# Optimization experiments

Hardware: AMD Instinct MI355X
Metric: run time of the kernel (lower is better)

## Reference

```python
import jax, jax.numpy as jnp
import numpy as np

DIM = 1024
NUM_HEADS = 16
HEAD_DIM = DIM // NUM_HEADS
SCALE = HEAD_DIM ** -0.5


def setup_inputs() -> dict:
    key = jax.random.key(0)
    k1, k2, k3 = jax.random.split(key, 3)
    B, N = 2, 2048
    x = jax.random.normal(k1, (B, N, DIM), dtype=jnp.float32)
    W_qkv = jax.random.normal(k2, (DIM, 3 * DIM), dtype=jnp.float32) * (DIM ** -0.5)
    b_qkv = jnp.zeros((3 * DIM,), dtype=jnp.float32)
    W_proj = jax.random.normal(k3, (DIM, DIM), dtype=jnp.float32) * (DIM ** -0.5)
    b_proj = jnp.zeros((DIM,), dtype=jnp.float32)
    return {"x": x, "W_qkv": W_qkv, "b_qkv": b_qkv, "W_proj": W_proj, "b_proj": b_proj}


def reference(x, W_qkv, b_qkv, W_proj, b_proj):
    B, N, D = x.shape
    qkv = x @ W_qkv + b_qkv                      # [B, N, 3D]
    qkv = qkv.reshape(B, N, 3, NUM_HEADS, HEAD_DIM)
    qkv = jnp.transpose(qkv, (2, 0, 3, 1, 4))    # [3, B, H, N, hd]
    q, k, v = qkv[0], qkv[1], qkv[2]
    attn = jnp.einsum('bhqd,bhkd->bhqk', q, k) * SCALE  # [B, H, N, N]
    attn = jax.nn.softmax(attn, axis=-1)
    out = jnp.einsum('bhqk,bhkd->bhqd', attn, v)        # [B, H, N, hd]
    out = jnp.transpose(out, (0, 2, 1, 3)).reshape(B, N, D)
    out = out @ W_proj + b_proj
    return out
```

## Files before the change

kernel.cpp:

```cpp
#include <hip/hip_runtime.h>


typedef __bf16 bf16_t;
typedef __bf16 bf16x2 __attribute__((ext_vector_type(2)));
typedef __bf16 bf16x4 __attribute__((ext_vector_type(4)));
typedef __bf16 bf16x8 __attribute__((ext_vector_type(8)));
typedef float  f32x4  __attribute__((ext_vector_type(4)));

#define NTOK 2048
#define DIM  1024
#define NH   16
#define HD   64
#define SCL2 0.18033688011112042f

#define MFMA16(a, b, c) __builtin_amdgcn_mfma_f32_16x16x32_bf16((a), (b), (c), 0, 0, 0)
#define BAR()   __builtin_amdgcn_s_barrier()
#define LGKM0() asm volatile("s_waitcnt lgkmcnt(0)" ::: "memory")

__device__ __forceinline__ void gload_lds16(const void* g, void* l) {
  __builtin_amdgcn_global_load_lds((const __attribute__((address_space(1))) void*)g,
                                   (__attribute__((address_space(3))) void*)l, 16, 0, 0);
}

__device__ __forceinline__ void transpose_cvt_tile(const float* __restrict__ W,
                                                   bf16_t* __restrict__ WT,
                                                   int cols, int bx, int by) {
  __shared__ float tile[32][33];
  int j0 = bx * 32, i0 = by * 32;
  int c = threadIdx.x & 31, r0 = threadIdx.x >> 5;
#pragma unroll
  for (int it = 0; it < 4; ++it) {
    int r = r0 + it * 8;
    tile[r][c] = W[(long)(i0 + r) * cols + j0 + c];
  }
  __syncthreads();
#pragma unroll
  for (int it = 0; it < 4; ++it) {
    int r = r0 + it * 8;
    int orow = j0 + r, ocol = i0 + c;
    WT[(long)orow * 1024 + ((((ocol >> 3) ^ (orow & 7)) << 3) | (ocol & 7))] =
        (bf16_t)tile[c][r];
  }
}

__global__ __launch_bounds__(256) void k_prep(const float* __restrict__ x,
                                              bf16_t* __restrict__ xb,
                                              const float* __restrict__ Wq,
                                              bf16_t* __restrict__ WqT,
                                              const float* __restrict__ Wp,
                                              bf16_t* __restrict__ WpT) {
  int id = blockIdx.x;
  if (id < 2048) {
    int i = (id * 256 + threadIdx.x) * 8;
    float4 a = *(const float4*)(x + i);
    float4 b = *(const float4*)(x + i + 4);
    bf16x8 v;
    v[0] = (bf16_t)a.x; v[1] = (bf16_t)a.y; v[2] = (bf16_t)a.z; v[3] = (bf16_t)a.w;
    v[4] = (bf16_t)b.x; v[5] = (bf16_t)b.y; v[6] = (bf16_t)b.z; v[7] = (bf16_t)b.w;
    int r = i >> 10, c = (i & 1023) >> 3;
    *(bf16x8*)(xb + r * 1024 + ((c ^ (r & 7)) << 3)) = v;
  } else if (id < 2048 + 3072) {
    int t = id - 2048;
    transpose_cvt_tile(Wq, WqT, 3072, t % 96, t / 96);
  } else {
    int t = id - 5120;
    transpose_cvt_tile(Wp, WpT, 1024, t & 31, t >> 5);
  }
}

__global__ __launch_bounds__(512, 2) void k_gemm_qkv(const bf16_t* __restrict__ xb,
                                                     const bf16_t* __restrict__ WqT,
                                                     const float* __restrict__ bq,
                                                     bf16_t* __restrict__ Qb,
                                                     bf16_t* __restrict__ Kb,
                                                     bf16_t* __restrict__ Vt) {
  __shared__ alignas(16) bf16_t SH[65536];
  const int t = threadIdx.x;
  const int w = t >> 6, lane = t & 63;
  const int l15 = lane & 15, g = lane >> 4;
  const int wm = w >> 2, wn = w & 3;
  const int xr = l15 & 7;

  const int bid = blockIdx.x;
  const int xcd = bid & 7, ib = bid >> 3;
  const int bm = ((xcd & 3) * 4 + (ib & 3)) * 256;
  const int bn = ((xcd >> 2) * 6 + (ib >> 2)) * 256;

  const bf16_t* Ag = xb + (long)bm * 1024;
  const bf16_t* Bg = WqT + (long)bn * 1024;

  auto Asl = [&](int slot) -> bf16_t* { return SH + slot * 16384; };
  auto Bsl = [&](int slot) -> bf16_t* { return SH + 32768 + slot * 16384; };

  auto st1 = [&](bf16_t* lds, const bf16_t* gsrc, int row0, int kt) {
    gload_lds16(gsrc + (long)(row0 + (t >> 3)) * 1024 + kt * 64 + (t & 7) * 8,
                (char*)lds + row0 * 128 + t * 16);
  };
  auto evA = [&](int slot, int kt, int half) {
    st1(Asl(slot), Ag, half * 64, kt);
    st1(Asl(slot), Ag, half * 64 + 128, kt);
  };
  auto evB = [&](int slot, int kt, int half) {
    st1(Bsl(slot), Bg, half * 128, kt);
    st1(Bsl(slot), Bg, half * 128 + 64, kt);
  };

  f32x4 acc[8][4];
  const f32x4 vzero = {0.f, 0.f, 0.f, 0.f};
#pragma unroll
  for (int m = 0; m < 8; ++m)
#pragma unroll
    for (int n = 0; n < 4; ++n) acc[m][n] = vzero;

  bf16x8 bf[4][2], af[4][2];
  auto ldB2 = [&](int slot, int n0) {
#pragma unroll
    for (int n = n0; n < n0 + 2; ++n)
#pragma unroll
      for (int kk = 0; kk < 2; ++kk)
        bf[n][kk] = *(const bf16x8*)((const char*)Bsl(slot) +
                    (wn * 64 + n * 16 + l15) * 128 + (((kk * 4 + g) ^ xr) << 4));
  };
  auto ldA = [&](int slot, int half) {
#pragma unroll
    for (int m = 0; m < 4; ++m)
#pragma unroll
      for (int kk = 0; kk < 2; ++kk)
        af[m][kk] = *(const bf16x8*)((const char*)Asl(slot) +
                    (wm * 128 + half * 64 + m * 16 + l15) * 128 +
                    (((kk * 4 + g) ^ xr) << 4));
  };
  auto mma = [&](int mb, int nb) {
    __builtin_amdgcn_s_setprio(1);
#pragma unroll
    for (int m = 0; m < 4; ++m)
#pragma unroll
      for (int n = 0; n < 2; ++n)
#pragma unroll
        for (int kk = 0; kk < 2; ++kk)
          acc[mb + m][nb + n] = MFMA16(af[m][kk], bf[nb + n][kk], acc[mb + m][nb + n]);
    __builtin_amdgcn_s_setprio(0);
  };

  evB(0, 0, 0); evB(0, 0, 1); evA(0, 0, 0); evA(0, 0, 1);
  evB(1, 1, 0); evB(1, 1, 1); evA(1, 1, 0); evA(1, 1, 1);
  asm volatile("s_waitcnt vmcnt(8)" ::: "memory");
  BAR();

  for (int T = 0; T < 16; ++T) {
    const int h = T & 1;
    const bool stg = (T + 2) < 16;
    ldB2(h, 0); ldA(h, 0);
    BAR(); LGKM0();
    mma(0, 0);
    BAR();
    ldB2(h, 2);
    BAR(); LGKM0();
    mma(0, 2);
    BAR();
    ldA(h, 1);
    if (stg) { evB(h, T + 2, 0); evB(h, T + 2, 1); }
    BAR(); LGKM0();
    mma(4, 0);
    BAR();
    if (stg) {
      evA(h, T + 2, 0); evA(h, T + 2, 1);
      asm volatile("s_waitcnt vmcnt(8)" ::: "memory");
    } else {
      asm volatile("s_waitcnt vmcnt(0)" ::: "memory");
    }
    BAR();
    mma(4, 2);
    BAR();
  }

  const int t3 = bn >> 10;
  const int h0 = (bn & 1023) >> 6;
  const int bb = bm >> 11;
  const int tok0 = bm & 2047;
  {
    const int region = wn * 16384;
#pragma unroll
    for (int n = 0; n < 4; ++n) {
      int d = n * 16 + l15;
      float bias = bq[bn + wn * 64 + n * 16 + l15];
#pragma unroll
      for (int m = 0; m < 8; ++m) {
#pragma unroll
        for (int r = 0; r < 4; ++r) {
          int ltok = wm * 128 + m * 16 + g * 4 + r;
          float val = acc[m][n][r] + bias;
          int off;
          if (t3 == 0) {
            off = ltok * 64 + d;
            val *= SCL2;
          } else if (t3 == 1) {
            int rr = ltok & 63;
            off = (ltok >> 6) * 4096 + rr * 64 + (((d >> 3) ^ (rr & 7)) << 3) + (d & 7);
          } else {
            int ct = ltok & 63;
            off = (ltok >> 6) * 4096 + d * 64 + (((ct >> 3) ^ (d & 7)) << 3) + (ct & 7);
          }
          SH[region + off] = (bf16_t)val;
        }
      }
    }
  }
  BAR();
  bf16_t* dst = (t3 == 0) ? Qb : (t3 == 1 ? Kb : Vt);
  const long tilebase = (t3 == 0) ? (long)tok0 * HD : (long)(tok0 >> 6) * 4096;
#pragma unroll
  for (int hl = 0; hl < 4; ++hl) {
    long gbase = (long)(bb * NH + h0 + hl) * (NTOK * HD) + tilebase;
#pragma unroll
    for (int p = 0; p < 4; ++p) {
      bf16x8 vv = *(const bf16x8*)(SH + hl * 16384 + p * 4096 + t * 8);
      *(bf16x8*)(dst + gbase + p * 4096 + t * 8) = vv;
    }
  }
}

__device__ __forceinline__ void gemm_core(const bf16_t* __restrict__ A,
                                          const bf16_t* __restrict__ B,
                                          int K, int bm, int bn,
                                          bf16_t* As, bf16_t* Bs, f32x4 acc[4][4]) {
  const int t = threadIdx.x;
  const int lane = t & 63;
  const int w = t >> 6;
  const int wr = (w >> 1) * 64, wc = (w & 1) * 64;
  const int l15 = lane & 15, g = lane >> 4;
  const int srow = t >> 3, scol = (t & 7) * 8;
  const f32x4 vzero = {0.f, 0.f, 0.f, 0.f};
#pragma unroll
  for (int m = 0; m < 4; ++m)
#pragma unroll
    for (int n = 0; n < 4; ++n) acc[m][n] = vzero;

  const bf16_t* ga = A + (long)(bm + srow) * K + scol;
  const bf16_t* gb = B + (long)(bn + srow) * K + scol;
  bf16_t* lA = As + srow * 64 + scol;
  bf16_t* lB = Bs + srow * 64 + scol;
  const int xr = l15 & 7;

  auto stageAB = [&](int buf, int k0) {
#pragma unroll
    for (int j = 0; j < 4; ++j) {
      gload_lds16(ga + (long)32 * j * K + k0, lA + buf * 8192 + j * 2048);
      gload_lds16(gb + (long)32 * j * K + k0, lB + buf * 8192 + j * 2048);
    }
  };

  const int nsteps = K >> 6;
  stageAB(0, 0);
  stageAB(1, 64);

  for (int s = 0; s < nsteps; ++s) {
    if (s == nsteps - 1) asm volatile("s_waitcnt vmcnt(0)" ::: "memory");
    else                 asm volatile("s_waitcnt vmcnt(8)" ::: "memory");
    __builtin_amdgcn_s_barrier();
    const char* Ab = (const char*)(As + (s & 1) * 8192);
    const char* Bb = (const char*)(Bs + (s & 1) * 8192);
#pragma unroll
    for (int kk = 0; kk < 2; ++kk) {
      bf16x8 af[4], bfv[4];
#pragma unroll
      for (int m = 0; m < 4; ++m)
        af[m] = *(const bf16x8*)(Ab + (wr + m * 16 + l15) * 128 +
                                 (((kk * 4 + g) ^ xr) << 4));
#pragma unroll
      for (int n = 0; n < 4; ++n)
        bfv[n] = *(const bf16x8*)(Bb + (wc + n * 16 + l15) * 128 +
                                  (((kk * 4 + g) ^ xr) << 4));
#pragma unroll
      for (int m = 0; m < 4; ++m)
#pragma unroll
        for (int n = 0; n < 4; ++n)
          acc[m][n] = MFMA16(af[m], bfv[n], acc[m][n]);
    }
    __builtin_amdgcn_s_barrier();
    if (s + 2 < nsteps) stageAB(s & 1, (s + 2) * 64);
  }
}

__global__ __launch_bounds__(256, 3) void k_attn(const bf16_t* __restrict__ Qb,
                                                 const bf16_t* __restrict__ Kb,
                                                 const bf16_t* __restrict__ Vt,
                                                 bf16_t* __restrict__ Ob) {
  __shared__ alignas(16) bf16_t Ks[2][64 * 64];
  __shared__ alignas(16) bf16_t Vs[2][64 * 64];
  __shared__ alignas(16) char  P2[4][4096];

  const int b0 = blockIdx.x;
  const int swz = (b0 & 7) * 64 + (b0 >> 3);
  const int qt = swz & 15, bh = swz >> 4;
  const int b = bh >> 4, h = bh & 15;
  const int t = threadIdx.x;
  const int w = t >> 6, lane = t & 63;
  const int l15 = lane & 15, g = lane >> 4;
  const bf16_t* Qp = Qb + bh * (NTOK * HD);
  const bf16_t* Kp = Kb + bh * (NTOK * HD);
  const bf16_t* Vp = Vt + bh * (NTOK * HD);
  const int q0 = qt * 128 + w * 32;
  char* P2w = &P2[w][0];

  const int cs0 = ((g ^ (l15 & 7)) << 4);
  const int cs1 = cs0 ^ 64;

  bf16x8 qfr[2][2];
#pragma unroll
  for (int qf = 0; qf < 2; ++qf)
#pragma unroll
    for (int kk = 0; kk < 2; ++kk)
      qfr[qf][kk] = *(const bf16x8*)(Qp + (q0 + qf * 16 + l15) * HD + kk * 32 + g * 8);

  bf16x8 ones;
#pragma unroll
  for (int i = 0; i < 8; ++i) ones[i] = (bf16_t)1.0f;

  const f32x4 vzero = {0.f, 0.f, 0.f, 0.f};
  f32x4 o[2][4];
#pragma unroll
  for (int qf = 0; qf < 2; ++qf)
#pragma unroll
    for (int df = 0; df < 4; ++df) o[qf][df] = vzero;
  f32x4 o_sum[2] = {vzero, vzero};

  auto stage = [&](int buf, int tile) {
    const bf16_t* gk = Kp + tile * 4096 + t * 8;
    const bf16_t* gv = Vp + tile * 4096 + t * 8;
    gload_lds16(gk,        (char*)Ks[buf] + t * 16);
    gload_lds16(gk + 2048, (char*)Ks[buf] + 4096 + t * 16);
    gload_lds16(gv,        (char*)Vs[buf] + t * 16);
    gload_lds16(gv + 2048, (char*)Vs[buf] + 4096 + t * 16);
  };

  stage(0, 0);
  stage(1, 1);

  for (int i = 0; i < 32; ++i) {
    if (i == 31) asm volatile("s_waitcnt vmcnt(0)" ::: "memory");
    else         asm volatile("s_waitcnt vmcnt(4)" ::: "memory");
    __builtin_amdgcn_s_barrier();
    const char* kbuf = (const char*)Ks[i & 1];
    const char* vbuf = (const char*)Vs[i & 1];
    f32x4 s[2][4];
    __builtin_amdgcn_s_setprio(1);
#pragma unroll
    for (int kf = 0; kf < 4; ++kf) {
      int rb = (kf * 16 + l15) * 128;
      bf16x8 ka0 = *(const bf16x8*)(kbuf + rb + cs0);
      bf16x8 ka1 = *(const bf16x8*)(kbuf + rb + cs1);
      s[0][kf] = MFMA16(ka0, qfr[0][0], vzero);
      s[1][kf] = MFMA16(ka0, qfr[1][0], vzero);
      s[0][kf] = MFMA16(ka1, qfr[0][1], s[0][kf]);
      s[1][kf] = MFMA16(ka1, qfr[1][1], s[1][kf]);
    }
    __builtin_amdgcn_s_setprio(0);
#pragma unroll
    for (int qf = 0; qf < 2; ++qf)
#pragma unroll
      for (int kf = 0; kf < 4; ++kf) {
        bf16x4 pw;
        pw[0] = (bf16_t)__builtin_amdgcn_exp2f(s[qf][kf][0]);
        pw[1] = (bf16_t)__builtin_amdgcn_exp2f(s[qf][kf][1]);
        pw[2] = (bf16_t)__builtin_amdgcn_exp2f(s[qf][kf][2]);
        pw[3] = (bf16_t)__builtin_amdgcn_exp2f(s[qf][kf][3]);
        *(bf16x4*)(P2w + qf * 2048 + (2 * kf + (g >> 1)) * 256 + l15 * 16 + 8 * (g & 1)) = pw;
      }
    __builtin_amdgcn_s_setprio(1);
#pragma unroll
    for (int kb = 0; kb < 2; ++kb) {
      bf16x8 pf0 = *(const bf16x8*)(P2w + kb * 1024 + lane * 16);
      bf16x8 pf1 = *(const bf16x8*)(P2w + 2048 + kb * 1024 + lane * 16);
      int csk = kb ? cs1 : cs0;
      o_sum[0] = MFMA16(ones, pf0, o_sum[0]);
      o_sum[1] = MFMA16(ones, pf1, o_sum[1]);
#pragma unroll
      for (int df = 0; df < 4; ++df) {
        bf16x8 va = *(const bf16x8*)(vbuf + (df * 16 + l15) * 128 + csk);
        o[0][df] = MFMA16(va, pf0, o[0][df]);
        o[1][df] = MFMA16(va, pf1, o[1][df]);
      }
    }
    __builtin_amdgcn_s_setprio(0);
    __builtin_amdgcn_s_barrier();
    if (i + 2 < 32) stage(i & 1, i + 2);
  }
#pragma unroll
  for (int qf = 0; qf < 2; ++qf) {
    float inv = 1.0f / o_sum[qf][0];
    int tok = q0 + qf * 16 + l15;
    bf16_t* oprow = Ob + (long)(b * NTOK + tok) * DIM;
    const int xr = l15 & 7;
#pragma unroll
    for (int df = 0; df < 4; ++df) {
#pragma unroll
      for (int rp = 0; rp < 2; ++rp) {
        bf16x2 v2;
        v2[0] = (bf16_t)(o[qf][df][rp * 2]     * inv);
        v2[1] = (bf16_t)(o[qf][df][rp * 2 + 1] * inv);
        int c = h * 8 + df * 2 + (g >> 1);
        *(bf16x2*)(oprow + ((c ^ xr) << 3) + (g & 1) * 4 + rp * 2) = v2;
      }
    }
  }
}

__global__ __launch_bounds__(256) void k_gemm_proj(const bf16_t* __restrict__ Ob,
                                                   const bf16_t* __restrict__ WpT,
                                                   const float* __restrict__ bp,
                                                   float* __restrict__ out) {
  __shared__ alignas(16) bf16_t As[2 * 128 * 64];
  __shared__ alignas(16) bf16_t Bs[2 * 128 * 64];
  f32x4 acc[4][4];
  const int bid = blockIdx.x;
  const int bn = (bid & 7) * 128;
  const int bm = (bid >> 3) * 128;
  gemm_core(Ob, WpT, DIM, bm, bn, As, Bs, acc);

  const int lane = threadIdx.x & 63, w = threadIdx.x >> 6;
  const int wr = (w >> 1) * 64, wc = (w & 1) * 64;
  const int l15 = lane & 15, g = lane >> 4;
#pragma unroll
  for (int n = 0; n < 4; ++n) {
    int col = bn + wc + n * 16 + l15;
    float bias = bp[col];
#pragma unroll
    for (int m = 0; m < 4; ++m) {
      int rowb = bm + wr + m * 16 + g * 4;
#pragma unroll
      for (int r = 0; r < 4; ++r)
        out[(long)(rowb + r) * DIM + col] = acc[m][n][r] + bias;
    }
  }
}

extern "C" void kernel_launch(void* const* d_in, const int* in_sizes, int n_in,
                              void* d_out, int out_size, void* d_ws, size_t ws_size,
                              hipStream_t stream) {
  const float* x     = (const float*)d_in[0];
  const float* Wqkv  = (const float*)d_in[1];
  const float* bqkv  = (const float*)d_in[2];
  const float* Wproj = (const float*)d_in[3];
  const float* bproj = (const float*)d_in[4];
  float* out = (float*)d_out;

  char* ws = (char*)d_ws;
  bf16_t* xb  = (bf16_t*)(ws);
  bf16_t* WqT = (bf16_t*)(ws + (8l  << 20));
  bf16_t* WpT = (bf16_t*)(ws + (14l << 20));
  bf16_t* Qb  = (bf16_t*)(ws + (16l << 20));
  bf16_t* Kb  = (bf16_t*)(ws + (24l << 20));
  bf16_t* Vt  = (bf16_t*)(ws + (32l << 20));
  bf16_t* Ob  = (bf16_t*)(ws);

  k_prep<<<6144, 256, 0, stream>>>(x, xb, Wqkv, WqT, Wproj, WpT);
  k_gemm_qkv<<<192, 512, 0, stream>>>(xb, WqT, bqkv, Qb, Kb, Vt);
  k_attn<<<512, 256, 0, stream>>>(Qb, Kb, Vt, Ob);
  k_gemm_proj<<<256, 256, 0, stream>>>(Ob, WpT, bproj, out);
}
```

Baseline: 112.5 us.

## Retile QKV GEMM to 256x192 blocks for 256 workgroups across CUs

Changes the QKV projection GEMM tile from 256x256 to 256x192 so the grid grows from 192 to 256 workgroups, filling all 256 CUs in one wave instead of leaving some idle. The B tile shrinks to three 64-row chunks. The A prefetch is split into two halves issued at different points in the loop, with matching vmcnt waits. The epilogue now works out the Q/K/V target and head per 64-column sub-tile, since a 192-wide tile can span multiple heads and tensors. The trade-off is lower arithmetic intensity per block and a more intricate prefetch schedule.

```diff
diff --git a/kernel.cpp b/kernel.cpp
--- a/kernel.cpp
+++ b/kernel.cpp
@@ -74,7 +74,7 @@
                                                      bf16_t* __restrict__ Qb,
                                                      bf16_t* __restrict__ Kb,
                                                      bf16_t* __restrict__ Vt) {
-  __shared__ alignas(16) bf16_t SH[65536];
+  __shared__ alignas(16) bf16_t SH[57344];
   const int t = threadIdx.x;
   const int w = t >> 6, lane = t & 63;
   const int l15 = lane & 15, g = lane >> 4;
@@ -84,42 +84,45 @@
   const int bid = blockIdx.x;
   const int xcd = bid & 7, ib = bid >> 3;
   const int bm = ((xcd & 3) * 4 + (ib & 3)) * 256;
-  const int bn = ((xcd >> 2) * 6 + (ib >> 2)) * 256;
+  const int bn = ((xcd >> 2) * 8 + (ib >> 2)) * 192;
 
   const bf16_t* Ag = xb + (long)bm * 1024;
   const bf16_t* Bg = WqT + (long)bn * 1024;
 
   auto Asl = [&](int slot) -> bf16_t* { return SH + slot * 16384; };
-  auto Bsl = [&](int slot) -> bf16_t* { return SH + 32768 + slot * 16384; };
+  auto Bsl = [&](int slot) -> bf16_t* { return SH + 32768 + slot * 12288; };
 
   auto st1 = [&](bf16_t* lds, const bf16_t* gsrc, int row0, int kt) {
     gload_lds16(gsrc + (long)(row0 + (t >> 3)) * 1024 + kt * 64 + (t & 7) * 8,
                 (char*)lds + row0 * 128 + t * 16);
   };
-  auto evA = [&](int slot, int kt, int half) {
-    st1(Asl(slot), Ag, half * 64, kt);
-    st1(Asl(slot), Ag, half * 64 + 128, kt);
-  };
-  auto evB = [&](int slot, int kt, int half) {
-    st1(Bsl(slot), Bg, half * 128, kt);
-    st1(Bsl(slot), Bg, half * 128 + 64, kt);
-  };
-
-  f32x4 acc[8][4];
+  auto evA0 = [&](int slot, int kt) {
+    st1(Asl(slot), Ag, 0, kt);
+    st1(Asl(slot), Ag, 128, kt);
+  };
+  auto evA1 = [&](int slot, int kt) {
+    st1(Asl(slot), Ag, 64, kt);
+    st1(Asl(slot), Ag, 192, kt);
+  };
+  auto evB = [&](int slot, int kt) {
+    st1(Bsl(slot), Bg, 0, kt);
+    st1(Bsl(slot), Bg, 64, kt);
+    st1(Bsl(slot), Bg, 128, kt);
+  };
+
+  f32x4 acc[8][3];
   const f32x4 vzero = {0.f, 0.f, 0.f, 0.f};
 #pragma unroll
   for (int m = 0; m < 8; ++m)
 #pragma unroll
-    for (int n = 0; n < 4; ++n) acc[m][n] = vzero;
-
-  bf16x8 bf[4][2], af[4][2];
-  auto ldB2 = [&](int slot, int n0) {
-#pragma unroll
-    for (int n = n0; n < n0 + 2; ++n)
-#pragma unroll
-      for (int kk = 0; kk < 2; ++kk)
-        bf[n][kk] = *(const bf16x8*)((const char*)Bsl(slot) +
-                    (wn * 64 + n * 16 + l15) * 128 + (((kk * 4 + g) ^ xr) << 4));
+    for (int n = 0; n < 3; ++n) acc[m][n] = vzero;
+
+  bf16x8 bf[3][2], af[4][2];
+  auto ldBn = [&](int slot, int n) {
+#pragma unroll
+    for (int kk = 0; kk < 2; ++kk)
+      bf[n][kk] = *(const bf16x8*)((const char*)Bsl(slot) +
+                  (wn * 48 + n * 16 + l15) * 128 + (((kk * 4 + g) ^ xr) << 4));
   };
   auto ldA = [&](int slot, int half) {
 #pragma unroll
@@ -130,7 +133,7 @@
                     (wm * 128 + half * 64 + m * 16 + l15) * 128 +
                     (((kk * 4 + g) ^ xr) << 4));
   };
-  auto mma = [&](int mb, int nb) {
+  auto mma2 = [&](int mb) {
     __builtin_amdgcn_s_setprio(1);
 #pragma unroll
     for (int m = 0; m < 4; ++m)
@@ -138,80 +141,92 @@
       for (int n = 0; n < 2; ++n)
 #pragma unroll
         for (int kk = 0; kk < 2; ++kk)
-          acc[mb + m][nb + n] = MFMA16(af[m][kk], bf[nb + n][kk], acc[mb + m][nb + n]);
+          acc[mb + m][n] = MFMA16(af[m][kk], bf[n][kk], acc[mb + m][n]);
     __builtin_amdgcn_s_setprio(0);
   };
-
-  evB(0, 0, 0); evB(0, 0, 1); evA(0, 0, 0); evA(0, 0, 1);
-  evB(1, 1, 0); evB(1, 1, 1); evA(1, 1, 0); evA(1, 1, 1);
-  asm volatile("s_waitcnt vmcnt(8)" ::: "memory");
+  auto mma1 = [&](int mb) {
+    __builtin_amdgcn_s_setprio(1);
+#pragma unroll
+    for (int m = 0; m < 4; ++m)
+#pragma unroll
+      for (int kk = 0; kk < 2; ++kk)
+        acc[mb + m][2] = MFMA16(af[m][kk], bf[2][kk], acc[mb + m][2]);
+    __builtin_amdgcn_s_setprio(0);
+  };
+
+  evB(0, 0); evA0(0, 0); evA1(0, 0);
+  evB(1, 1); evA0(1, 1);
+  asm volatile("s_waitcnt vmcnt(5)" ::: "memory");
   BAR();
 
   for (int T = 0; T < 16; ++T) {
     const int h = T & 1;
     const bool stg = (T + 2) < 16;
-    ldB2(h, 0); ldA(h, 0);
+    if (T + 1 < 16) evA1(h ^ 1, T + 1);
+    ldBn(h, 0); ldBn(h, 1); ldA(h, 0);
     BAR(); LGKM0();
-    mma(0, 0);
+    mma2(0);
     BAR();
-    ldB2(h, 2);
+    ldBn(h, 2);
     BAR(); LGKM0();
-    mma(0, 2);
+    mma1(0);
     BAR();
     ldA(h, 1);
-    if (stg) { evB(h, T + 2, 0); evB(h, T + 2, 1); }
+    if (stg) evB(h, T + 2);
     BAR(); LGKM0();
-    mma(4, 0);
+    mma2(4);
     BAR();
     if (stg) {
-      evA(h, T + 2, 0); evA(h, T + 2, 1);
-      asm volatile("s_waitcnt vmcnt(8)" ::: "memory");
+      evA0(h, T + 2);
+      asm volatile("s_waitcnt vmcnt(5)" ::: "memory");
     } else {
       asm volatile("s_waitcnt vmcnt(0)" ::: "memory");
     }
     BAR();
-    mma(4, 2);
+    mma1(4);
     BAR();
   }
 
-  const int t3 = bn >> 10;
-  const int h0 = (bn & 1023) >> 6;
   const int bb = bm >> 11;
   const int tok0 = bm & 2047;
-  {
-    const int region = wn * 16384;
-#pragma unroll
-    for (int n = 0; n < 4; ++n) {
-      int d = n * 16 + l15;
-      float bias = bq[bn + wn * 64 + n * 16 + l15];
-#pragma unroll
-      for (int m = 0; m < 8; ++m) {
-#pragma unroll
-        for (int r = 0; r < 4; ++r) {
-          int ltok = wm * 128 + m * 16 + g * 4 + r;
-          float val = acc[m][n][r] + bias;
-          int off;
-          if (t3 == 0) {
-            off = ltok * 64 + d;
-            val *= SCL2;
-          } else if (t3 == 1) {
-            int rr = ltok & 63;
-            off = (ltok >> 6) * 4096 + rr * 64 + (((d >> 3) ^ (rr & 7)) << 3) + (d & 7);
-          } else {
-            int ct = ltok & 63;
-            off = (ltok >> 6) * 4096 + d * 64 + (((ct >> 3) ^ (d & 7)) << 3) + (ct & 7);
-          }
-          SH[region + off] = (bf16_t)val;
+#pragma unroll
+  for (int n = 0; n < 3; ++n) {
+    int lc = wn * 48 + n * 16 + l15;
+    int col = bn + lc;
+    int t3 = col >> 10;
+    int d = col & 63;
+    int region = lc >> 6;
+    float bias = bq[col];
+#pragma unroll
+    for (int m = 0; m < 8; ++m) {
+#pragma unroll
+      for (int r = 0; r < 4; ++r) {
+        int ltok = wm * 128 + m * 16 + g * 4 + r;
+        float val = acc[m][n][r] + bias;
+        int off;
+        if (t3 == 0) {
+          off = ltok * 64 + d;
+          val *= SCL2;
+        } else if (t3 == 1) {
+          int rr = ltok & 63;
+          off = (ltok >> 6) * 4096 + rr * 64 + (((d >> 3) ^ (rr & 7)) << 3) + (d & 7);
+        } else {
+          int ct = ltok & 63;
+          off = (ltok >> 6) * 4096 + d * 64 + (((ct >> 3) ^ (d & 7)) << 3) + (ct & 7);
         }
+        SH[region * 16384 + off] = (bf16_t)val;
       }
     }
   }
   BAR();
-  bf16_t* dst = (t3 == 0) ? Qb : (t3 == 1 ? Kb : Vt);
-  const long tilebase = (t3 == 0) ? (long)tok0 * HD : (long)(tok0 >> 6) * 4096;
-#pragma unroll
-  for (int hl = 0; hl < 4; ++hl) {
-    long gbase = (long)(bb * NH + h0 + hl) * (NTOK * HD) + tilebase;
+#pragma unroll
+  for (int hl = 0; hl < 3; ++hl) {
+    int col0 = bn + hl * 64;
+    int t3 = col0 >> 10;
+    int hh = (col0 >> 6) & 15;
+    bf16_t* dst = (t3 == 0) ? Qb : (t3 == 1 ? Kb : Vt);
+    long tilebase = (t3 == 0) ? (long)tok0 * HD : (long)(tok0 >> 6) * 4096;
+    long gbase = (long)(bb * NH + hh) * (NTOK * HD) + tilebase;
 #pragma unroll
     for (int p = 0; p < 4; ++p) {
       bf16x8 vv = *(const bf16x8*)(SH + hl * 16384 + p * 4096 + t * 8);
@@ -455,7 +470,7 @@
   bf16_t* Ob  = (bf16_t*)(ws);
 
   k_prep<<<6144, 256, 0, stream>>>(x, xb, Wqkv, WqT, Wproj, WpT);
-  k_gemm_qkv<<<192, 512, 0, stream>>>(xb, WqT, bqkv, Qb, Kb, Vt);
+  k_gemm_qkv<<<256, 512, 0, stream>>>(xb, WqT, bqkv, Qb, Kb, Vt);
   k_attn<<<512, 256, 0, stream>>>(Qb, Kb, Vt, Ob);
   k_gemm_proj<<<256, 256, 0, stream>>>(Ob, WpT, bproj, out);
 }
```

Measured after the change: 105.3 us. -6.4%, faster.
